# Kernel optimization log

Measured on AMD Instinct MI355X. Metric: run time of the kernel, lower is better.

Reference implementation:

```python
import jax, jax.numpy as jnp
import numpy as np

G, S, D, L, H, NTASK = 128, 32, 128, 3, 4, 10
N = S                      # nodes per subgraph == subgraphs per graph (node-based policy)
T = G * S * N              # total nodes in batched subgraph graph
TO = G * N                 # total original nodes
E, EO = 1048576, 16384
EPS = 1e-5
HD = D // H


def setup_inputs() -> dict:
    key = jax.random.key(0)
    ks = jax.random.split(key, 24)
    nrm = lambda i, shape: jax.random.normal(ks[i], shape, dtype=jnp.float32) * 0.05
    return {
        "x": jax.random.normal(ks[0], (T, D), dtype=jnp.float32),
        "edge_index": jax.random.randint(ks[1], (2, E), 0, T, dtype=jnp.int32),
        "original_edge_index": jax.random.randint(ks[2], (2, EO), 0, TO, dtype=jnp.int32),
        "Wr1": nrm(3, (L, D, D)), "Wn1": nrm(4, (L, D, D)), "b1": nrm(5, (L, D)),
        "g1": jnp.ones((L, D), jnp.float32), "be1": jnp.zeros((L, D), jnp.float32),
        "Wr2": nrm(6, (L, D, D)), "Wn2": nrm(7, (L, D, D)), "b2": nrm(8, (L, D)),
        "g2": jnp.ones((L, D), jnp.float32), "be2": jnp.zeros((L, D), jnp.float32),
        "Wq": nrm(9, (L, D, D)), "bq": nrm(10, (L, D)),
        "Wk": nrm(11, (L, D, D)), "bk": nrm(12, (L, D)),
        "Wf1": nrm(13, (D, 2 * D)), "bf1": nrm(14, (2 * D,)),
        "Wf2": nrm(15, (2 * D, NTASK)), "bf2": nrm(16, (NTASK,)),
    }


def _bn(h, gamma, beta):
    mu = h.mean(0)
    var = h.var(0)  # biased, as torch BatchNorm1d (training)
    return gamma * (h - mu) * jax.lax.rsqrt(var + EPS) + beta


def _conv(h, src, dst, Wr, Wn, b, n_nodes):
    # GraphConv: root transform + sum-aggregated neighbor transform
    agg = jax.ops.segment_sum(h[src], dst, num_segments=n_nodes)
    return h @ Wr + agg @ Wn + b


def reference(x, edge_index, original_edge_index, Wr1, Wn1, b1, g1, be1,
              Wr2, Wn2, b2, g2, be2, Wq, bq, Wk, bk, Wf1, bf1, Wf2, bf2):
    src, dst = edge_index[0], edge_index[1]
    osrc, odst = original_edge_index[0], original_edge_index[1]
    scale = 1.0 / jnp.sqrt(jnp.float32(HD))
    attn = None
    for i in range(L):
        # subgraph-level GNN branch
        h1 = _bn(_conv(x, src, dst, Wr1[i], Wn1[i], b1[i], T), g1[i], be1[i])
        # scatter-mean nodes -> subgraph features: [G, S, D]
        sub = x.reshape(G, S, N, D).mean(axis=2)
        # block-diagonal masked MHA == per-graph attention (uniform blocks of S)
        q = (sub @ Wq[i] + bq[i]).reshape(G, S, H, HD)
        k = (sub @ Wk[i] + bk[i]).reshape(G, S, H, HD)
        scores = jnp.einsum("gihd,gjhd->ghij", q, k) * scale
        attn = jax.nn.softmax(scores, axis=-1).mean(axis=1)  # head-averaged, [G, S, S]
        # per-graph weighted reassembly: out[g, n] = sum_s attn[g, s, n] * x[g, s, n]
        xg = x.reshape(G, S, N, D)
        x_atten = jnp.einsum("gsn,gsnd->gnd", attn, xg).reshape(TO, D)
        # original-graph GNN branch
        h2 = _bn(_conv(x_atten, osrc, odst, Wr2[i], Wn2[i], b2[i], TO), g2[i], be2[i])
        # broadcast h2 back to subgraph nodes: node (g, s, n) <- h2[g*N + n]
        h2b = jnp.broadcast_to(h2.reshape(G, 1, N, D), (G, S, N, D)).reshape(T, D)
        x = jax.nn.relu(h1 + h2b)
    # subgraph mean-pool then graph mean over subgraphs
    h_graph = x.reshape(G, S, N, D).mean(axis=2).mean(axis=1)  # [G, D]
    logits = jax.nn.relu(h_graph @ Wf1 + bf1) @ Wf2 + bf2
    heatmap = attn[-1]  # last graph's attention block from last layer
    return logits, heatmap
```

## Files before the change

### kernel.cpp

```cpp
#include <hip/hip_runtime.h>

#define G_   128
#define S_   32
#define N_   32
#define D_   128
#define T_   (G_*S_*N_)
#define TO_  (G_*N_)
#define E_   1048576
#define EO_  16384
#define NTASK_ 10
#define CAP_ 32

typedef _Float16 h16;
typedef _Float16 half8 __attribute__((ext_vector_type(8)));
typedef _Float16 half4 __attribute__((ext_vector_type(4)));
typedef float f32x16 __attribute__((ext_vector_type(16)));

__global__ __launch_bounds__(256) void k_prep(
    const int* __restrict__ ei, const int* __restrict__ oei,
    const float* __restrict__ Wr1, const float* __restrict__ Wn1,
    const float* __restrict__ Wr2, const float* __restrict__ Wn2,
    const float* __restrict__ Wq, const float* __restrict__ Wk,
    const float* __restrict__ x0,
    int* __restrict__ cnt, int* __restrict__ ocnt,
    int* __restrict__ colsrc, int* __restrict__ ocolsrc,
    h16* __restrict__ wt, h16* __restrict__ wqkt,
    h16* __restrict__ xh, h16* __restrict__ subh)
{
    __shared__ float red[8][132];
    int b = blockIdx.x, t = threadIdx.x;
    if (b < 8192) {
        const int p = b & 7;
        const int e0 = (b >> 3) * 1024 + t * 4;
        const int4 d4 = *(const int4*)&ei[E_ + e0];
        const int4 s4 = *(const int4*)&ei[e0];
        #pragma unroll
        for (int j = 0; j < 4; ++j) {
            int d = (&d4.x)[j];
            if ((d >> 14) == p) {
                int pos = atomicAdd(&cnt[d], 1);
                if (pos < CAP_) colsrc[(d << 5) + pos] = (&s4.x)[j];
            }
        }
    } else if (b < 8208) {
        const int e0 = (b - 8192) * 1024 + t * 4;
        const int4 d4 = *(const int4*)&oei[EO_ + e0];
        const int4 s4 = *(const int4*)&oei[e0];
        #pragma unroll
        for (int j = 0; j < 4; ++j) {
            int d = (&d4.x)[j];
            int pos = atomicAdd(&ocnt[d], 1);
            if (pos < CAP_) ocolsrc[(d << 5) + pos] = (&s4.x)[j];
        }
    } else if (b < 8400) {
        int idx = b - 8208, mat = idx >> 4, chunk = idx & 15;
        int arr = mat / 3, layer = mat % 3;
        const float* W = (arr == 0 ? Wr1 : arr == 1 ? Wn1 : arr == 2 ? Wr2 : Wn2) + (size_t)layer * 16384;
        h16* outh = wt + (size_t)mat * 32768;
        h16* outl = outh + 16384;
        int base = chunk * 1024;
        for (int i = t; i < 1024; i += 256) {
            int id = base + i;
            int k = id >> 7, n = id & 127;
            float v = W[id];
            h16 hi = (h16)v;
            h16 lo = (h16)(v - (float)hi);
            outh[n * 128 + k] = hi;
            outl[n * 128 + k] = lo;
        }
    } else if (b < 8496) {
        int idx = b - 8400, m = idx >> 4, chunk = idx & 15;
        int layer = m >> 1, which = m & 1;
        const float* W = (which ? Wk : Wq) + (size_t)layer * 16384;
        h16* o = wqkt + (size_t)m * 16384;
        int base = chunk * 1024;
        for (int i = t; i < 1024; i += 256) {
            int id = base + i;
            int k = id >> 7, n = id & 127;
            o[n * 128 + k] = (h16)W[id];
        }
    } else {
        int gs = b - 8496;
        int cg = t & 31, rg = t >> 5;
        int c4 = cg * 4;
        float4 ssum = make_float4(0.f, 0.f, 0.f, 0.f);
        for (int n = rg; n < 32; n += 8) {
            size_t tt = (size_t)gs * 32 + n;
            float4 v = *(const float4*)&x0[tt * 128 + c4];
            half4 o; o[0] = (h16)v.x; o[1] = (h16)v.y; o[2] = (h16)v.z; o[3] = (h16)v.w;
            *(half4*)&xh[tt * 128 + c4] = o;
            ssum.x += v.x; ssum.y += v.y; ssum.z += v.z; ssum.w += v.w;
        }
        *(float4*)&red[rg][c4] = ssum;
        __syncthreads();
        if (rg == 0) {
            float4 s = make_float4(0.f, 0.f, 0.f, 0.f);
            #pragma unroll
            for (int r = 0; r < 8; ++r) {
                float4 v = *(float4*)&red[r][c4];
                s.x += v.x; s.y += v.y; s.z += v.z; s.w += v.w;
            }
            const float inv = 1.f / 32.f;
            half4 o; o[0] = (h16)(s.x*inv); o[1] = (h16)(s.y*inv); o[2] = (h16)(s.z*inv); o[3] = (h16)(s.w*inv);
            *(half4*)&subh[(size_t)gs * 128 + c4] = o;
        }
    }
}

__global__ __launch_bounds__(256) void k_agg2(
    const h16* __restrict__ xh, const int* __restrict__ cnt, const int* __restrict__ colsrc,
    h16* __restrict__ agg)
{
    const int nid = blockIdx.x * 32 + (threadIdx.x >> 3);
    const int foff = blockIdx.y * 64 + (threadIdx.x & 7) * 8;
    int n = cnt[nid]; n = (n > CAP_) ? CAP_ : n;
    const int* __restrict__ bucket = colsrc + ((size_t)nid << 5);
    float acc[8] = {0.f,0.f,0.f,0.f,0.f,0.f,0.f,0.f};
    for (int e = 0; e < n; e += 4) {
        int4 s4 = *(const int4*)&bucket[e];
        #pragma unroll
        for (int j = 0; j < 4; ++j) {
            bool ok = (e + j) < n;
            int s = ok ? (&s4.x)[j] : 0;
            half8 v = *(const half8*)&xh[(size_t)s * 128 + foff];
            if (ok) {
                #pragma unroll
                for (int q = 0; q < 8; ++q) acc[q] += (float)v[q];
            }
        }
    }
    half8 o;
    #pragma unroll
    for (int j = 0; j < 8; ++j) o[j] = (h16)acc[j];
    *(half8*)&agg[(size_t)nid * 128 + foff] = o;
}

__global__ __launch_bounds__(256) void k_attn(
    const h16* __restrict__ subh, const h16* __restrict__ wqkt_l,
    const float* __restrict__ bql, const float* __restrict__ bkl,
    const h16* __restrict__ xh, float* __restrict__ heat, h16* __restrict__ xat)
{
    __shared__ __align__(16) char smem[25600];
    const int tid = threadIdx.x;
    const int g = blockIdx.x;
    h16* aF = (h16*)smem;
    h16* qkT = (h16*)(smem + 8192);
    float* attn_s = (float*)smem;
    #pragma unroll
    for (int it = 0; it < 2; ++it) {
        int u = tid + it * 256;
        int kq = u >> 6, l = u & 63;
        int m = l & 31, ko = kq * 16 + (l >> 5) * 8;
        *(half8*)&aF[u * 8] = *(const half8*)&subh[((size_t)g * 32 + m) * 128 + ko];
    }
    __syncthreads();
    const int w = tid >> 6, lane = tid & 63, lm = lane & 31, lh = lane >> 5;
    const int mat = w & 1, ntp = (w >> 1) * 2;
    const h16* Wt = wqkt_l + (size_t)mat * 16384;
    const float* bias = mat ? bkl : bql;
    f32x16 a0, a1;
    #pragma unroll
    for (int r = 0; r < 16; ++r) { a0[r] = 0.f; a1[r] = 0.f; }
    #pragma unroll
    for (int kq = 0; kq < 8; ++kq) {
        half8 av = *(half8*)&aF[(kq * 64 + lane) * 8];
        half8 b0 = *(const half8*)&Wt[(size_t)(ntp * 32 + lm) * 128 + kq * 16 + lh * 8];
        half8 b1 = *(const half8*)&Wt[(size_t)((ntp + 1) * 32 + lm) * 128 + kq * 16 + lh * 8];
        a0 = __builtin_amdgcn_mfma_f32_32x32x16_f16(av, b0, a0, 0, 0, 0);
        a1 = __builtin_amdgcn_mfma_f32_32x32x16_f16(av, b1, a1, 0, 0, 0);
    }
    __syncthreads();
    #pragma unroll
    for (int ti = 0; ti < 2; ++ti) {
        int n = (ntp + ti) * 32 + lm;
        float bn = bias[n];
        #pragma unroll
        for (int r = 0; r < 16; ++r) {
            int s = (r & 3) + 8 * (r >> 2) + 4 * lh;
            float v = (ti ? a1[r] : a0[r]) + bn;
            qkT[(mat * 128 + n) * 34 + s] = (h16)v;
        }
    }
    for (int i = tid; i < 1024; i += 256) attn_s[i] = 0.f;
    __syncthreads();
    if (tid < 128) {
        int h = tid >> 5, i = tid & 31;
        float qreg[32];
        #pragma unroll
        for (int d = 0; d < 32; ++d) qreg[d] = (float)qkT[(h * 32 + d) * 34 + i];
        float sc[32];
        const float scale = 0.17677669529663687f;
        float mx = -1e30f;
        #pragma unroll
        for (int j = 0; j < 32; ++j) {
            float d = 0.f;
            #pragma unroll
            for (int d0 = 0; d0 < 32; ++d0) d += qreg[d0] * (float)qkT[(128 + h * 32 + d0) * 34 + j];
            d *= scale;
            sc[j] = d;
            mx = fmaxf(mx, d);
        }
        float ssum = 0.f;
        #pragma unroll
        for (int j = 0; j < 32; ++j) { float ee = __expf(sc[j] - mx); sc[j] = ee; ssum += ee; }
        float inv = 0.25f / ssum;
        #pragma unroll
        for (int j = 0; j < 32; ++j) atomicAdd(&attn_s[i * 32 + j], sc[j] * inv);
    }
    __syncthreads();
    if (heat != nullptr && g == 127) {
        for (int idx = tid; idx < 1024; idx += 256) heat[idx] = attn_s[idx];
    }
    {
        int c4 = (tid & 31) * 4;
        int ng = tid >> 5;
        for (int n = ng; n < 32; n += 8) {
            float ax = 0.f, ay = 0.f, az = 0.f, aw = 0.f;
            #pragma unroll
            for (int s = 0; s < 32; ++s) {
                float a = attn_s[s * 32 + n];
                half4 xv = *(const half4*)&xh[(((size_t)g * 32 + s) * 32 + n) * 128 + c4];
                ax += a * (float)xv[0]; ay += a * (float)xv[1];
                az += a * (float)xv[2]; aw += a * (float)xv[3];
            }
            half4 o; o[0] = (h16)ax; o[1] = (h16)ay; o[2] = (h16)az; o[3] = (h16)aw;
            *(half4*)&xat[((size_t)g * 32 + n) * 128 + c4] = o;
        }
    }
}

__global__ __launch_bounds__(256) void k_aggo(
    const h16* __restrict__ x, const int* __restrict__ ocnt, const int* __restrict__ ocolsrc,
    h16* __restrict__ agg)
{
    int nid = blockIdx.x * 8 + (threadIdx.x >> 5);
    int lane = threadIdx.x & 31;
    int n = ocnt[nid]; n = (n > CAP_) ? CAP_ : n;
    const int* __restrict__ bucket = ocolsrc + ((size_t)nid << 5);
    float ax = 0.f, ay = 0.f, az = 0.f, aw = 0.f;
    for (int e = 0; e < n; e += 4) {
        int4 s4 = *(const int4*)&bucket[e];
        #pragma unroll
        for (int j = 0; j < 4; ++j) {
            bool ok = (e + j) < n;
            int s = ok ? (&s4.x)[j] : 0;
            half4 v = *(const half4*)&x[(size_t)s * 128 + lane * 4];
            if (ok) { ax += (float)v[0]; ay += (float)v[1]; az += (float)v[2]; aw += (float)v[3]; }
        }
    }
    half4 o; o[0] = (h16)ax; o[1] = (h16)ay; o[2] = (h16)az; o[3] = (h16)aw;
    *(half4*)&agg[(size_t)nid * 128 + lane * 4] = o;
}

__global__ __launch_bounds__(256) void k_convs(
    const h16* __restrict__ xT, const h16* __restrict__ aggT,
    const h16* __restrict__ xO, const h16* __restrict__ aggO,
    const h16* __restrict__ wt, int layer,
    const float* __restrict__ b1l, const float* __restrict__ b2l,
    h16* __restrict__ h1, h16* __restrict__ h2, float* __restrict__ stats)
{
    __shared__ h16 lsA[4096];
    __shared__ h16 lsBh[4096];
    __shared__ h16 lsBl[4096];
    __shared__ float csum[128], csq[128];
    const int tid = threadIdx.x;
    const h16 *A0, *A1, *W0, *W1; const float* bias; h16* outp; float *gsum, *gsq; size_t row0;
    if (blockIdx.x < 1024) {
        A0 = xT; A1 = aggT;
        W0 = wt + (size_t)(0 * 3 + layer) * 32768;
        W1 = wt + (size_t)(1 * 3 + layer) * 32768;
        bias = b1l; outp = h1; gsum = stats; gsq = stats + 128;
        row0 = (size_t)blockIdx.x * 128;
    } else {
        A0 = xO; A1 = aggO;
        W0 = wt + (size_t)(2 * 3 + layer) * 32768;
        W1 = wt + (size_t)(3 * 3 + layer) * 32768;
        bias = b2l; outp = h2; gsum = stats + 256; gsq = stats + 384;
        row0 = (size_t)(blockIdx.x - 1024) * 128;
    }
    if (tid < 128) { csum[tid] = 0.f; csq[tid] = 0.f; }
    const int w = tid >> 6, lane = tid & 63, lm = lane & 31, lh = lane >> 5;
    const int mbase = (w & 1) * 64, nbase = (w >> 1) * 64;
    f32x16 acc[2][2];
    #pragma unroll
    for (int mi = 0; mi < 2; ++mi)
        #pragma unroll
        for (int ni = 0; ni < 2; ++ni)
            #pragma unroll
            for (int r = 0; r < 16; ++r) acc[mi][ni][r] = 0.f;

    for (int p = 0; p < 2; ++p) {
        const h16* A  = p ? A1 : A0;
        const h16* Bh = p ? W1 : W0;
        const h16* Bl = Bh + 16384;
        for (int kc = 0; kc < 4; ++kc) {
            __syncthreads();
            #pragma unroll
            for (int it = 0; it < 2; ++it) {
                int u = tid + it * 256;
                int m = u & 127, ch = u >> 7;
                *(half8*)&lsA[u * 8]  = *(const half8*)&A[(row0 + m) * 128 + kc * 32 + ch * 8];
                *(half8*)&lsBh[u * 8] = *(const half8*)&Bh[(size_t)m * 128 + kc * 32 + ch * 8];
                *(half8*)&lsBl[u * 8] = *(const half8*)&Bl[(size_t)m * 128 + kc * 32 + ch * 8];
            }
            __syncthreads();
            #pragma unroll
            for (int c = 0; c < 2; ++c) {
                const int base = (2 * c + lh) * 128;
                half8 a0  = *(half8*)&lsA[(base + mbase + lm) * 8];
                half8 a1  = *(half8*)&lsA[(base + mbase + 32 + lm) * 8];
                half8 bh0 = *(half8*)&lsBh[(base + nbase + lm) * 8];
                half8 bh1 = *(half8*)&lsBh[(base + nbase + 32 + lm) * 8];
                half8 bl0 = *(half8*)&lsBl[(base + nbase + lm) * 8];
                half8 bl1 = *(half8*)&lsBl[(base + nbase + 32 + lm) * 8];
                acc[0][0] = __builtin_amdgcn_mfma_f32_32x32x16_f16(a0, bh0, acc[0][0], 0, 0, 0);
                acc[0][0] = __builtin_amdgcn_mfma_f32_32x32x16_f16(a0, bl0, acc[0][0], 0, 0, 0);
                acc[0][1] = __builtin_amdgcn_mfma_f32_32x32x16_f16(a0, bh1, acc[0][1], 0, 0, 0);
                acc[0][1] = __builtin_amdgcn_mfma_f32_32x32x16_f16(a0, bl1, acc[0][1], 0, 0, 0);
                acc[1][0] = __builtin_amdgcn_mfma_f32_32x32x16_f16(a1, bh0, acc[1][0], 0, 0, 0);
                acc[1][0] = __builtin_amdgcn_mfma_f32_32x32x16_f16(a1, bl0, acc[1][0], 0, 0, 0);
                acc[1][1] = __builtin_amdgcn_mfma_f32_32x32x16_f16(a1, bh1, acc[1][1], 0, 0, 0);
                acc[1][1] = __builtin_amdgcn_mfma_f32_32x32x16_f16(a1, bl1, acc[1][1], 0, 0, 0);
            }
        }
    }
    #pragma unroll
    for (int ni = 0; ni < 2; ++ni) {
        int col = nbase + ni * 32 + lm;
        float bcol = bias[col];
        float s = 0.f, q = 0.f;
        #pragma unroll
        for (int mi = 0; mi < 2; ++mi) {
            #pragma unroll
            for (int r = 0; r < 16; ++r) {
                int row = mbase + mi * 32 + (r & 3) + 8 * (r >> 2) + 4 * lh;
                float o = acc[mi][ni][r] + bcol;
                outp[(row0 + row) * 128 + col] = (h16)o;
                s += o; q += o * o;
            }
        }
        atomicAdd(&csum[col], s);
        atomicAdd(&csq[col], q);
    }
    __syncthreads();
    if (tid < 128) atomicAdd(&gsum[tid], csum[tid]);
    else           atomicAdd(&gsq[tid - 128], csq[tid - 128]);
}

__global__ __launch_bounds__(256) void k_update(
    const h16* __restrict__ hpre, const h16* __restrict__ h2pre,
    const float* __restrict__ stats,
    const float* __restrict__ g1, const float* __restrict__ be1,
    const float* __restrict__ g2, const float* __restrict__ be2,
    h16* __restrict__ x, h16* __restrict__ subh)
{
    __shared__ float sA[128], hA[128], sB[128], hB[128];
    __shared__ float red[8][132];
    int gs = blockIdx.x, g = gs >> 5, tid = threadIdx.x;
    if (tid < 128) {
        float mu = stats[tid] * (1.f / T_);
        float var = stats[128 + tid] * (1.f / T_) - mu * mu;
        float sc = g1[tid] * rsqrtf(var + 1e-5f);
        sA[tid] = sc; hA[tid] = be1[tid] - mu * sc;
    } else {
        int c = tid - 128;
        float mu = stats[256 + c] * (1.f / TO_);
        float var = stats[384 + c] * (1.f / TO_) - mu * mu;
        float sc = g2[c] * rsqrtf(var + 1e-5f);
        sB[c] = sc; hB[c] = be2[c] - mu * sc;
    }
    __syncthreads();
    int cg = tid & 31, ng = tid >> 5;
    int c4 = cg * 4;
    float4 ssum = make_float4(0.f, 0.f, 0.f, 0.f);
    for (int n = ng; n < 32; n += 8) {
        size_t t = (size_t)gs * 32 + n;
        half4 h1v = *(const half4*)&hpre[t * 128 + c4];
        half4 h2v = *(const half4*)&h2pre[((size_t)g * 32 + n) * 128 + c4];
        float o0 = fmaxf((float)h1v[0] * sA[c4+0] + hA[c4+0] + (float)h2v[0] * sB[c4+0] + hB[c4+0], 0.f);
        float o1 = fmaxf((float)h1v[1] * sA[c4+1] + hA[c4+1] + (float)h2v[1] * sB[c4+1] + hB[c4+1], 0.f);
        float o2 = fmaxf((float)h1v[2] * sA[c4+2] + hA[c4+2] + (float)h2v[2] * sB[c4+2] + hB[c4+2], 0.f);
        float o3 = fmaxf((float)h1v[3] * sA[c4+3] + hA[c4+3] + (float)h2v[3] * sB[c4+3] + hB[c4+3], 0.f);
        half4 o; o[0] = (h16)o0; o[1] = (h16)o1; o[2] = (h16)o2; o[3] = (h16)o3;
        *(half4*)&x[t * 128 + c4] = o;
        ssum.x += o0; ssum.y += o1; ssum.z += o2; ssum.w += o3;
    }
    *(float4*)&red[ng][c4] = ssum;
    __syncthreads();
    if (ng == 0) {
        float4 s = make_float4(0.f, 0.f, 0.f, 0.f);
        #pragma unroll
        for (int r = 0; r < 8; ++r) {
            float4 v = *(float4*)&red[r][c4];
            s.x += v.x; s.y += v.y; s.z += v.z; s.w += v.w;
        }
        const float inv = 1.f / 32.f;
        half4 o; o[0] = (h16)(s.x*inv); o[1] = (h16)(s.y*inv); o[2] = (h16)(s.z*inv); o[3] = (h16)(s.w*inv);
        *(half4*)&subh[(size_t)gs * 128 + c4] = o;
    }
}

__global__ __launch_bounds__(256) void k_dense(const h16* __restrict__ subh, const float* __restrict__ Wf1,
    const float* __restrict__ bf1, const float* __restrict__ Wf2, const float* __restrict__ bf2,
    float* __restrict__ out)
{
    int g = blockIdx.x, tid = threadIdx.x;
    __shared__ float hgs[128];
    __shared__ float hid[256];
    if (tid < 128) {
        float s = 0.f;
        for (int ss = 0; ss < 32; ++ss) s += (float)subh[((size_t)g * 32 + ss) * 128 + tid];
        hgs[tid] = s * (1.f / 32.f);
    }
    __syncthreads();
    float a = bf1[tid];
    for (int k = 0; k < 128; ++k) a += hgs[k] * Wf1[k * 256 + tid];
    hid[tid] = fmaxf(a, 0.f);
    __syncthreads();
    if (tid < 10) {
        float o = bf2[tid];
        for (int k = 0; k < 256; ++k) o += hid[k] * Wf2[k * 10 + tid];
        out[g * 10 + tid] = o;
    }
}

extern "C" void kernel_launch(void* const* d_in, const int* in_sizes, int n_in,
                              void* d_out, int out_size, void* d_ws, size_t ws_size,
                              hipStream_t stream)
{
    (void)in_sizes; (void)n_in; (void)out_size; (void)ws_size;
    const float* x0  = (const float*)d_in[0];
    const int*   ei  = (const int*)d_in[1];
    const int*   oei = (const int*)d_in[2];
    const float* Wr1 = (const float*)d_in[3];
    const float* Wn1 = (const float*)d_in[4];
    const float* b1  = (const float*)d_in[5];
    const float* g1  = (const float*)d_in[6];
    const float* be1 = (const float*)d_in[7];
    const float* Wr2 = (const float*)d_in[8];
    const float* Wn2 = (const float*)d_in[9];
    const float* b2  = (const float*)d_in[10];
    const float* g2  = (const float*)d_in[11];
    const float* be2 = (const float*)d_in[12];
    const float* Wq  = (const float*)d_in[13];
    const float* bq  = (const float*)d_in[14];
    const float* Wk  = (const float*)d_in[15];
    const float* bk  = (const float*)d_in[16];
    const float* Wf1 = (const float*)d_in[17];
    const float* bf1 = (const float*)d_in[18];
    const float* Wf2 = (const float*)d_in[19];
    const float* bf2 = (const float*)d_in[20];
    float* out = (float*)d_out;

    char* w = (char*)d_ws;
    size_t off = 0;
    auto alloc = [&](size_t bytes) { void* p = w + off; off = (off + bytes + 255) & ~(size_t)255; return p; };
    h16* xh     = (h16*)alloc((size_t)T_ * D_ * 2);
    h16* aggh   = (h16*)alloc((size_t)T_ * D_ * 2);
    h16* agg2   = (h16*)alloc((size_t)TO_ * D_ * 2);
    h16* xat    = (h16*)alloc((size_t)TO_ * D_ * 2);
    h16* wt     = (h16*)alloc((size_t)12 * 32768 * 2);
    h16* wqkt   = (h16*)alloc((size_t)6 * 16384 * 2);
    h16* subh   = (h16*)alloc((size_t)G_ * S_ * D_ * 2);
    int* cnt     = (int*)alloc((size_t)(T_ + TO_) * 4 + 1536 * 4);
    int* ocnt    = cnt + T_;
    float* stats = (float*)(cnt + T_ + TO_);
    int* colsrc  = (int*)alloc((size_t)T_ * CAP_ * 4);
    int* ocolsrc = (int*)alloc((size_t)TO_ * CAP_ * 4);

    h16* h1pre = aggh;
    h16* h2pre = agg2;

    hipMemsetAsync(cnt, 0, (size_t)(T_ + TO_) * 4 + 1536 * 4, stream);
    k_prep<<<12592, 256, 0, stream>>>(ei, oei, Wr1, Wn1, Wr2, Wn2, Wq, Wk, x0,
                                      cnt, ocnt, colsrc, ocolsrc, wt, wqkt, xh, subh);

    for (int i = 0; i < 3; ++i) {
        k_agg2<<<dim3(T_ / 32, 2), 256, 0, stream>>>(xh, cnt, colsrc, aggh);
        k_attn<<<G_, 256, 0, stream>>>(subh, wqkt + (size_t)i * 2 * 16384,
            bq + i * D_, bk + i * D_, xh,
            (i == 2) ? (out + G_ * NTASK_) : nullptr, xat);
        k_aggo<<<TO_ / 8, 256, 0, stream>>>(xat, ocnt, ocolsrc, agg2);
        k_convs<<<1056, 256, 0, stream>>>(xh, aggh, xat, agg2, wt, i,
            b1 + i * D_, b2 + i * D_, h1pre, h2pre, stats + i * 512);
        k_update<<<G_ * S_, 256, 0, stream>>>(h1pre, h2pre, stats + i * 512,
            g1 + i * D_, be1 + i * D_, g2 + i * D_, be2 + i * D_, xh, subh);
    }
    k_dense<<<G_, 256, 0, stream>>>(subh, Wf1, bf1, Wf2, bf2, out);
}
```

Baseline: 651.0 us.

## Drop partitioned edge scatter; load A tile via global_load_lds, B from global

```diff
diff --git a/kernel.cpp b/kernel.cpp
--- a/kernel.cpp
+++ b/kernel.cpp
@@ -29,21 +29,18 @@
 {
     __shared__ float red[8][132];
     int b = blockIdx.x, t = threadIdx.x;
-    if (b < 8192) {
-        const int p = b & 7;
-        const int e0 = (b >> 3) * 1024 + t * 4;
+    if (b < 1024) {
+        const int e0 = b * 1024 + t * 4;
         const int4 d4 = *(const int4*)&ei[E_ + e0];
         const int4 s4 = *(const int4*)&ei[e0];
         #pragma unroll
         for (int j = 0; j < 4; ++j) {
             int d = (&d4.x)[j];
-            if ((d >> 14) == p) {
-                int pos = atomicAdd(&cnt[d], 1);
-                if (pos < CAP_) colsrc[(d << 5) + pos] = (&s4.x)[j];
-            }
-        }
-    } else if (b < 8208) {
-        const int e0 = (b - 8192) * 1024 + t * 4;
+            int pos = atomicAdd(&cnt[d], 1);
+            if (pos < CAP_) colsrc[(d << 5) + pos] = (&s4.x)[j];
+        }
+    } else if (b < 1040) {
+        const int e0 = (b - 1024) * 1024 + t * 4;
         const int4 d4 = *(const int4*)&oei[EO_ + e0];
         const int4 s4 = *(const int4*)&oei[e0];
         #pragma unroll
@@ -52,8 +49,8 @@
             int pos = atomicAdd(&ocnt[d], 1);
             if (pos < CAP_) ocolsrc[(d << 5) + pos] = (&s4.x)[j];
         }
-    } else if (b < 8400) {
-        int idx = b - 8208, mat = idx >> 4, chunk = idx & 15;
+    } else if (b < 1232) {
+        int idx = b - 1040, mat = idx >> 4, chunk = idx & 15;
         int arr = mat / 3, layer = mat % 3;
         const float* W = (arr == 0 ? Wr1 : arr == 1 ? Wn1 : arr == 2 ? Wr2 : Wn2) + (size_t)layer * 16384;
         h16* outh = wt + (size_t)mat * 32768;
@@ -68,8 +65,8 @@
             outh[n * 128 + k] = hi;
             outl[n * 128 + k] = lo;
         }
-    } else if (b < 8496) {
-        int idx = b - 8400, m = idx >> 4, chunk = idx & 15;
+    } else if (b < 1328) {
+        int idx = b - 1232, m = idx >> 4, chunk = idx & 15;
         int layer = m >> 1, which = m & 1;
         const float* W = (which ? Wk : Wq) + (size_t)layer * 16384;
         h16* o = wqkt + (size_t)m * 16384;
@@ -80,7 +77,7 @@
             o[n * 128 + k] = (h16)W[id];
         }
     } else {
-        int gs = b - 8496;
+        int gs = b - 1328;
         int cg = t & 31, rg = t >> 5;
         int c4 = cg * 4;
         float4 ssum = make_float4(0.f, 0.f, 0.f, 0.f);
@@ -259,9 +256,7 @@
     const float* __restrict__ b1l, const float* __restrict__ b2l,
     h16* __restrict__ h1, h16* __restrict__ h2, float* __restrict__ stats)
 {
-    __shared__ h16 lsA[4096];
-    __shared__ h16 lsBh[4096];
-    __shared__ h16 lsBl[4096];
+    __shared__ __align__(16) h16 lsA[4096];
     __shared__ float csum[128], csq[128];
     const int tid = threadIdx.x;
     const h16 *A0, *A1, *W0, *W1; const float* bias; h16* outp; float *gsum, *gsq; size_t row0;
@@ -281,6 +276,8 @@
     if (tid < 128) { csum[tid] = 0.f; csq[tid] = 0.f; }
     const int w = tid >> 6, lane = tid & 63, lm = lane & 31, lh = lane >> 5;
     const int mbase = (w & 1) * 64, nbase = (w >> 1) * 64;
+    const int u_m0 = tid & 127, u_ch0 = tid >> 7;
+    const int u_m1 = tid & 127, u_ch1 = (tid >> 7) + 2;
     f32x16 acc[2][2];
     #pragma unroll
     for (int mi = 0; mi < 2; ++mi)
@@ -295,24 +292,29 @@
         const h16* Bl = Bh + 16384;
         for (int kc = 0; kc < 4; ++kc) {
             __syncthreads();
-            #pragma unroll
-            for (int it = 0; it < 2; ++it) {
-                int u = tid + it * 256;
-                int m = u & 127, ch = u >> 7;
-                *(half8*)&lsA[u * 8]  = *(const half8*)&A[(row0 + m) * 128 + kc * 32 + ch * 8];
-                *(half8*)&lsBh[u * 8] = *(const half8*)&Bh[(size_t)m * 128 + kc * 32 + ch * 8];
-                *(half8*)&lsBl[u * 8] = *(const half8*)&Bl[(size_t)m * 128 + kc * 32 + ch * 8];
+            {
+                const h16* g0 = &A[(row0 + u_m0) * 128 + kc * 32 + u_ch0 * 8];
+                const h16* g1 = &A[(row0 + u_m1) * 128 + kc * 32 + u_ch1 * 8];
+                h16* l0 = &lsA[(size_t)((0 * 256 + (tid & ~63)) * 8)];
+                h16* l1 = &lsA[(size_t)((1 * 256 + (tid & ~63)) * 8)];
+                __builtin_amdgcn_global_load_lds(
+                    (const __attribute__((address_space(1))) void*)g0,
+                    (__attribute__((address_space(3))) void*)l0, 16, 0, 0);
+                __builtin_amdgcn_global_load_lds(
+                    (const __attribute__((address_space(1))) void*)g1,
+                    (__attribute__((address_space(3))) void*)l1, 16, 0, 0);
             }
             __syncthreads();
             #pragma unroll
             for (int c = 0; c < 2; ++c) {
                 const int base = (2 * c + lh) * 128;
+                const int koff = kc * 32 + (2 * c + lh) * 8;
                 half8 a0  = *(half8*)&lsA[(base + mbase + lm) * 8];
                 half8 a1  = *(half8*)&lsA[(base + mbase + 32 + lm) * 8];
-                half8 bh0 = *(half8*)&lsBh[(base + nbase + lm) * 8];
-                half8 bh1 = *(half8*)&lsBh[(base + nbase + 32 + lm) * 8];
-                half8 bl0 = *(half8*)&lsBl[(base + nbase + lm) * 8];
-                half8 bl1 = *(half8*)&lsBl[(base + nbase + 32 + lm) * 8];
+                half8 bh0 = *(const half8*)&Bh[(size_t)(nbase + lm) * 128 + koff];
+                half8 bh1 = *(const half8*)&Bh[(size_t)(nbase + 32 + lm) * 128 + koff];
+                half8 bl0 = *(const half8*)&Bl[(size_t)(nbase + lm) * 128 + koff];
+                half8 bl1 = *(const half8*)&Bl[(size_t)(nbase + 32 + lm) * 128 + koff];
                 acc[0][0] = __builtin_amdgcn_mfma_f32_32x32x16_f16(a0, bh0, acc[0][0], 0, 0, 0);
                 acc[0][0] = __builtin_amdgcn_mfma_f32_32x32x16_f16(a0, bl0, acc[0][0], 0, 0, 0);
                 acc[0][1] = __builtin_amdgcn_mfma_f32_32x32x16_f16(a0, bh1, acc[0][1], 0, 0, 0);
@@ -472,8 +474,8 @@
     h16* h2pre = agg2;
 
     hipMemsetAsync(cnt, 0, (size_t)(T_ + TO_) * 4 + 1536 * 4, stream);
-    k_prep<<<12592, 256, 0, stream>>>(ei, oei, Wr1, Wn1, Wr2, Wn2, Wq, Wk, x0,
-                                      cnt, ocnt, colsrc, ocolsrc, wt, wqkt, xh, subh);
+    k_prep<<<5424, 256, 0, stream>>>(ei, oei, Wr1, Wn1, Wr2, Wn2, Wq, Wk, x0,
+                                     cnt, ocnt, colsrc, ocolsrc, wt, wqkt, xh, subh);
 
     for (int i = 0; i < 3; ++i) {
         k_agg2<<<dim3(T_ / 32, 2), 256, 0, stream>>>(xh, cnt, colsrc, aggh);
```

Result: slower. 733.1 us (+12.6%).
